# Performance work log

Hardware: AMD Instinct MI355X
Metric: run time of the kernel (lower is better)

Reference implementation:

```python
import jax, jax.numpy as jnp
import numpy as np

HEADS = 8
DIM_HEAD = 64
QUERY_DIM = 320
INNER = HEADS * DIM_HEAD
B = 1
N = 2304          # 48*48 latent pixels
HS = WS = 48
SCALE = DIM_HEAD ** -0.5
ATTN_MATRIX_SCALE = 1.5   # injection_config['T']


def setup_inputs() -> dict:
    key = jax.random.key(0)
    ks = jax.random.split(key, 10)
    f = lambda k, s: jax.random.normal(k, s, dtype=jnp.float32)
    return {
        'x': f(ks[0], (B, N, QUERY_DIM)),
        'Wq': f(ks[1], (QUERY_DIM, INNER)) * 0.05,
        'Wo': f(ks[2], (INNER, QUERY_DIM)) * 0.05,
        'bo': jnp.zeros((QUERY_DIM,), jnp.float32),
        'q_injected': f(ks[3], (B * HEADS, N, DIM_HEAD)),
        'k_injected': f(ks[4], (B * HEADS, N, DIM_HEAD)),
        'v_injected': f(ks[5], (B * HEADS, N, DIM_HEAD)),
        'cnt_k_injected': f(ks[6], (B * HEADS, N, DIM_HEAD)),
        'cnt_v_injected': f(ks[7], (B * HEADS, N, DIM_HEAD)),
        'mask': jax.random.uniform(ks[8], (HS, WS), dtype=jnp.float32),
    }


def _split_heads(t):
    # 'b n (h d) -> (b h) n d'
    b, n, _ = t.shape
    return t.reshape(b, n, HEADS, DIM_HEAD).transpose(0, 2, 1, 3).reshape(b * HEADS, n, DIM_HEAD)


def reference(x, Wq, Wo, bo, q_injected, k_injected, v_injected,
              cnt_k_injected, cnt_v_injected, mask):
    # --- q/k/v with injection (b=1 so torch.cat([.]*b) is identity) ---
    q_in = q_injected                          # (bh, N, d)
    q_ = _split_heads(x @ Wq)                  # to_q(x) -> (bh, N, d)
    q = 0.5 * q_in + 0.5 * q_                  # blended query
    k = k_injected
    v = v_injected
    q_cnt, k_cnt, v_cnt = q_in, cnt_k_injected, cnt_v_injected

    # --- get_batch_sim: content-content similarity (b=1 => rearrange is identity) ---
    cc_sim = jnp.einsum('hid,hjd->hij', q_cnt, k_cnt) * SCALE     # (h, N, N)

    # --- get_batch_sim_with_mask ---
    sim = jnp.einsum('hid,hjd->hij', q, k) * (ATTN_MATRIX_SCALE * SCALE)  # (h, N, N)
    sim_r = sim.reshape(HEADS, HS, WS, N)
    cc_r = cc_sim.reshape(HEADS, HS, WS, N)
    max_sim = jnp.einsum('hid,hjd->hij', q_cnt, k)                # delta_q x delta_k (=self.k)
    max_sim_r = max_sim.reshape(HEADS, HS, WS, N)
    min_cc = jnp.min(cc_r, axis=3, keepdims=True)                 # (h, HS, WS, 1)
    max_ms = jnp.max(max_sim_r, axis=3, keepdims=True)            # (h, HS, WS, 1)

    # binary-threshold the mask, flip sign, bilinear-resize to (HS, WS)
    m = jnp.where(mask < 0.5, -1.0, jnp.where(mask > 0.5, 1.0, mask)) * -1.0
    m = jax.image.resize(m[None, None], (1, 1, HS, WS), method='bilinear')
    m = m.reshape(1, HS, WS, 1)

    gvm = (min_cc - max_ms) * m                                   # gradual_vanished_mask
    sim = (sim_r + gvm).reshape(HEADS, N, N)                      # rows [:WS] == all rows here

    # B=1 => the view/permute/reshape block is identity: sim, cc_sim are (h, N, N)
    # concatenated softmax over style keys and content keys
    cat_sim = jnp.concatenate([sim, cc_sim], axis=2)              # (h, N, 2N)
    cat_attn = jax.nn.softmax(cat_sim, axis=-1)
    cat_v = jnp.concatenate([v, v_cnt], axis=1)                   # (h, 2N, d)
    cat_out = jnp.einsum('hij,hjd->hid', cat_attn, cat_v)         # (h, N, d)

    # 'h (b n) d -> b n (h d)' with b=1
    out = cat_out.transpose(1, 0, 2).reshape(B, N, INNER)
    return out @ Wo + bo
```

## Files before the change

kernel.cpp:

```cpp
#include <hip/hip_runtime.h>
#include <math.h>

#define HEADS 8
#define NTOK  2304
#define DH    64
#define QD    320
#define INNER 512
#define TPS   36
#define PSTR  68

typedef _Float16 f16;
typedef f16  f16x4 __attribute__((ext_vector_type(4)));
typedef f16  f16x8 __attribute__((ext_vector_type(8)));
typedef float f32x4 __attribute__((ext_vector_type(4)));

#define MFMA(a,b,c) __builtin_amdgcn_mfma_f32_16x16x32_f16((a),(b),(c),0,0,0)

#define GLDS(gp, lp) __builtin_amdgcn_global_load_lds(                      \
    (const __attribute__((address_space(1))) void*)(gp),                    \
    (__attribute__((address_space(3))) void*)(lp), 16, 0, 0)

#if __has_builtin(__builtin_amdgcn_exp2f)
#define EXP2(x) __builtin_amdgcn_exp2f(x)
#else
#define EXP2(x) exp2f(x)
#endif

#define LOG2E 1.44269504f

static __device__ __forceinline__ unsigned pkrtz(float a, float b) {
#if __has_builtin(__builtin_amdgcn_cvt_pkrtz)
  return __builtin_bit_cast(unsigned, __builtin_amdgcn_cvt_pkrtz(a, b));
#else
  union { f16 h[2]; unsigned u; } c;
  c.h[0] = (f16)a; c.h[1] = (f16)b;
  return c.u;
#endif
}

__global__ __launch_bounds__(256) void prep_all(
    const float* __restrict__ qi, const float* __restrict__ ki,
    const float* __restrict__ kc, const float* __restrict__ x,
    const float* __restrict__ v,  const float* __restrict__ vc,
    const float* __restrict__ Wq, const float* __restrict__ Wo,
    f16* __restrict__ oq, f16* __restrict__ ok, f16* __restrict__ okc,
    f16* __restrict__ ox, f16* __restrict__ vt, f16* __restrict__ vct,
    f16* __restrict__ WqT, f16* __restrict__ WoT)
{
  __shared__ float T[64][65];
  const int bid = blockIdx.x;
  const int tid = threadIdx.x;

  if (bid < 2088) {
    int i = bid * 256 + tid;
    const float* src; f16* dst; float s = 1.0f; int off;
    if (i < 147456)      { src = qi; dst = oq;  off = i; }
    else if (i < 294912) { src = ki; dst = ok;  off = i - 147456; }
    else if (i < 442368) { src = kc; dst = okc; off = i - 294912; s = 0.125f * LOG2E; }
    else                 { src = x;  dst = ox;  off = i - 442368; }
    float4 a = reinterpret_cast<const float4*>(src)[off * 2];
    float4 b = reinterpret_cast<const float4*>(src)[off * 2 + 1];
    f16x8 o;
    o[0] = (f16)(a.x * s); o[1] = (f16)(a.y * s);
    o[2] = (f16)(a.z * s); o[3] = (f16)(a.w * s);
    o[4] = (f16)(b.x * s); o[5] = (f16)(b.y * s);
    o[6] = (f16)(b.z * s); o[7] = (f16)(b.w * s);
    *reinterpret_cast<f16x8*>(&dst[(size_t)off * 8]) = o;
  } else if (bid < 2664) {
    int t = bid - 2088;
    int z = t / 288, rem = t % 288;
    int h = rem / 36, nt = rem % 36;
    const float* src = z ? vc : v;
    f16* dst = z ? vct : vt;
    const int n0 = nt * 64;
    const size_t base = ((size_t)h * NTOK + n0) * DH;
    for (int it = 0; it < 4; ++it) {
      int idx = tid + it * 256;
      int n = idx >> 4, d0 = (idx & 15) * 4;
      float4 a = *reinterpret_cast<const float4*>(&src[base + (size_t)n * DH + d0]);
      T[n][d0] = a.x; T[n][d0 + 1] = a.y; T[n][d0 + 2] = a.z; T[n][d0 + 3] = a.w;
    }
    __syncthreads();
    for (int it = 0; it < 2; ++it) {
      int idx = tid + it * 256;
      int d = idx >> 3, c0 = (idx & 7) * 8;
      f16x8 o;
      #pragma unroll
      for (int i = 0; i < 8; ++i) o[i] = (f16)T[c0 + i][d];
      *reinterpret_cast<f16x8*>(&dst[(size_t)(h * 64 + d) * NTOK + n0 + c0]) = o;
    }
  } else {
    int t = bid - 2664;
    int z = t / 40, b = t % 40;
    const float* src = z ? Wo : Wq;
    f16* dst = z ? WoT : WqT;
    const int R = z ? INNER : QD;
    const int C = z ? QD : INNER;
    const int ctiles = C >> 6;
    const int rt = b / ctiles, ct = b % ctiles;
    for (int it = 0; it < 4; ++it) {
      int idx = tid + it * 256;
      int r = idx >> 4, c4 = (idx & 15) * 4;
      float4 a = *reinterpret_cast<const float4*>(&src[(size_t)(rt * 64 + r) * C + ct * 64 + c4]);
      T[r][c4] = a.x; T[r][c4 + 1] = a.y; T[r][c4 + 2] = a.z; T[r][c4 + 3] = a.w;
    }
    __syncthreads();
    for (int it = 0; it < 4; ++it) {
      int idx = tid + it * 256;
      int c = idx >> 4, r4 = (idx & 15) * 4;
      f16x4 o;
      #pragma unroll
      for (int i = 0; i < 4; ++i) o[i] = (f16)T[r4 + i][c];
      *reinterpret_cast<f16x4*>(&dst[(size_t)(ct * 64 + c) * R + rt * 64 + r4]) = o;
    }
  }
}

__global__ __launch_bounds__(256) void qblend_mfma(
    const f16* __restrict__ x16, const f16* __restrict__ WqT,
    const float* __restrict__ qinj, f16* __restrict__ qhat)
{
  const int qt = blockIdx.x, h = blockIdx.y;
  const int n0 = qt * 32;
  const int tid = threadIdx.x;
  const int w = tid >> 6, l = tid & 63, lq = l & 15, lk = l >> 4;
  const int qsub = w & 1, ch = w >> 1;
  f32x4 acc[2] = {};
  const f16* arow = x16 + (size_t)(n0 + qsub * 16 + lq) * QD;
  #pragma unroll
  for (int ks = 0; ks < 10; ++ks) {
    f16x8 a = *reinterpret_cast<const f16x8*>(&arow[ks * 32 + lk * 8]);
    #pragma unroll
    for (int df = 0; df < 2; ++df) {
      const f16* brow = WqT + (size_t)(h * 64 + ch * 32 + df * 16 + lq) * QD;
      f16x8 b = *reinterpret_cast<const f16x8*>(&brow[ks * 32 + lk * 8]);
      acc[df] = MFMA(a, b, acc[df]);
    }
  }
  const float sc = 0.09375f * LOG2E;
  #pragma unroll
  for (int df = 0; df < 2; ++df)
    #pragma unroll
    for (int r = 0; r < 4; ++r) {
      int n = n0 + qsub * 16 + lk * 4 + r;
      int d = ch * 32 + df * 16 + lq;
      size_t idx = ((size_t)h * NTOK + n) * DH + d;
      qhat[idx] = (f16)(sc * (qinj[idx] + acc[df][r]));
    }
}

__global__ __launch_bounds__(64) void attn_pw(
    const f16* __restrict__ qhat, const f16* __restrict__ qc16,
    const f16* __restrict__ k16,  const f16* __restrict__ kc16,
    const f16* __restrict__ vt16, const f16* __restrict__ vct16,
    float* __restrict__ part)
{
  __shared__ __align__(16) f16 smem[3][2][2048];
  __shared__ __align__(16) f16 pbuf[640];

  const int bid = blockIdx.x;
  const int h    = bid & 7;
  const int strm = (bid >> 3) & 1;
  const int sp   = (bid >> 4) & 1;
  const int wq   = bid >> 5;
  const int l = threadIdx.x;
  const int lq = l & 15, lk = l >> 4;
  const size_t hb = (size_t)h * NTOK * DH;
  const int row0 = wq * 48 + lq;

  f16x8 qh0[2], qh1[2], qh2[2], qc0[2], qc1[2], qc2[2];
  {
    const size_t qr0 = hb + (size_t)row0 * DH;
    #pragma unroll
    for (int ks = 0; ks < 2; ++ks) {
      const int o = ks * 32 + lk * 8;
      qc0[ks] = *reinterpret_cast<const f16x8*>(&qc16[qr0 + o]);
      qc1[ks] = *reinterpret_cast<const f16x8*>(&qc16[qr0 + 16 * DH + o]);
      qc2[ks] = *reinterpret_cast<const f16x8*>(&qc16[qr0 + 32 * DH + o]);
      if (!strm) {
        qh0[ks] = *reinterpret_cast<const f16x8*>(&qhat[qr0 + o]);
        qh1[ks] = *reinterpret_cast<const f16x8*>(&qhat[qr0 + 16 * DH + o]);
        qh2[ks] = *reinterpret_cast<const f16x8*>(&qhat[qr0 + 32 * DH + o]);
      } else { qh0[ks] = qc0[ks]; qh1[ks] = qc1[ks]; qh2[ks] = qc2[ks]; }
    }
  }

  const int ksw  = ((l & 7) ^ (l >> 3)) * 8;
  const int krw  = l >> 3;
  const int vrw  = l >> 2;
  const int voff = (l & 3) * 8;
  const f16* gK = (strm ? kc16 : k16) + hb;
  const f16* gV = (strm ? vct16 : vt16) + (size_t)h * DH * NTOK;

  #define STAGE(nb, j0)                                                       \
    do {                                                                      \
      _Pragma("unroll")                                                       \
      for (int c = 0; c < 4; ++c) {                                           \
        GLDS(gK + (size_t)((j0) + c * 8 + krw) * 64 + ksw,                    \
             &smem[nb][0][c * 512]);                                          \
        GLDS(gV + (size_t)(c * 16 + vrw) * NTOK + (j0) + voff,                \
             &smem[nb][1][c * 512]);                                          \
      }                                                                       \
    } while (0)

  const int swz = (lq & 7) * 8;
  int xo[2];
  #pragma unroll
  for (int ks = 0; ks < 2; ++ks) xo[ks] = ((ks * 32 + lk * 8) ^ swz);

  float S0 = 0.f, S1 = 0.f, S2 = 0.f;
  float ax0, ax1, ax2;
  ax0 = ax1 = ax2 = strm ? INFINITY : -INFINITY;
  f32x4 O0[4] = {}, O1_[4] = {}, O2_[4] = {};

  auto SMX = [&](const f32x4* s, float& Sl) -> f16x8 {
    float p0 = EXP2(s[0][0]), p1 = EXP2(s[0][1]);
    float p2 = EXP2(s[0][2]), p3 = EXP2(s[0][3]);
    float p4 = EXP2(s[1][0]), p5 = EXP2(s[1][1]);
    float p6 = EXP2(s[1][2]), p7 = EXP2(s[1][3]);
    Sl += ((p0 + p1) + (p2 + p3)) + ((p4 + p5) + (p6 + p7));
    uint2 wA, wB;
    wA.x = pkrtz(p0, p1); wA.y = pkrtz(p2, p3);
    wB.x = pkrtz(p4, p5); wB.y = pkrtz(p6, p7);
    *reinterpret_cast<uint2*>(pbuf + lq * 40 + lk * 4)      = wA;
    *reinterpret_cast<uint2*>(pbuf + lq * 40 + 16 + lk * 4) = wB;
    return *reinterpret_cast<const f16x8*>(pbuf + lq * 40 + lk * 8);
  };

  const int jb = sp * (TPS * 32);
  STAGE(0, jb);
  STAGE(1, jb + 32);

  for (int t = 0; t < TPS; ++t) {
    if (t + 2 < TPS) {
      STAGE((t + 2) % 3, jb + (t + 2) * 32);
      asm volatile("s_waitcnt vmcnt(16)" ::: "memory");
    } else if (t + 1 < TPS) {
      asm volatile("s_waitcnt vmcnt(8)" ::: "memory");
    } else {
      asm volatile("s_waitcnt vmcnt(0)" ::: "memory");
    }
    __builtin_amdgcn_sched_barrier(0);

    const int bi = t % 3;
    const f16* Kb = &smem[bi][0][0];
    const f16* Vb = &smem[bi][1][0];

    f32x4 sA[2] = {}, sB[2] = {}, sC[2] = {};
    __builtin_amdgcn_s_setprio(1);
    if (!strm) {
      float m3A = -INFINITY, m3B = -INFINITY, m3C = -INFINITY;
      #pragma unroll
      for (int jf = 0; jf < 2; ++jf) {
        f32x4 tA = {}, tB = {}, tC = {};
        const int rb = (jf * 16 + lq) * 64;
        #pragma unroll
        for (int ks = 0; ks < 2; ++ks) {
          f16x8 aK = *reinterpret_cast<const f16x8*>(&Kb[rb + xo[ks]]);
          sA[jf] = MFMA(aK, qh0[ks], sA[jf]);
          sB[jf] = MFMA(aK, qh1[ks], sB[jf]);
          sC[jf] = MFMA(aK, qh2[ks], sC[jf]);
          tA = MFMA(aK, qc0[ks], tA);
          tB = MFMA(aK, qc1[ks], tB);
          tC = MFMA(aK, qc2[ks], tC);
        }
        m3A = fmaxf(m3A, fmaxf(fmaxf(tA[0], tA[1]), fmaxf(tA[2], tA[3])));
        m3B = fmaxf(m3B, fmaxf(fmaxf(tB[0], tB[1]), fmaxf(tB[2], tB[3])));
        m3C = fmaxf(m3C, fmaxf(fmaxf(tC[0], tC[1]), fmaxf(tC[2], tC[3])));
      }
      ax0 = fmaxf(ax0, m3A); ax1 = fmaxf(ax1, m3B); ax2 = fmaxf(ax2, m3C);
    } else {
      #pragma unroll
      for (int jf = 0; jf < 2; ++jf) {
        const int rb = (jf * 16 + lq) * 64;
        #pragma unroll
        for (int ks = 0; ks < 2; ++ks) {
          f16x8 aK = *reinterpret_cast<const f16x8*>(&Kb[rb + xo[ks]]);
          sA[jf] = MFMA(aK, qc0[ks], sA[jf]);
          sB[jf] = MFMA(aK, qc1[ks], sB[jf]);
          sC[jf] = MFMA(aK, qc2[ks], sC[jf]);
        }
      }
      ax0 = fminf(ax0, fminf(fminf(fminf(sA[0][0], sA[0][1]), fminf(sA[0][2], sA[0][3])),
                             fminf(fminf(sA[1][0], sA[1][1]), fminf(sA[1][2], sA[1][3]))));
      ax1 = fminf(ax1, fminf(fminf(fminf(sB[0][0], sB[0][1]), fminf(sB[0][2], sB[0][3])),
                             fminf(fminf(sB[1][0], sB[1][1]), fminf(sB[1][2], sB[1][3]))));
      ax2 = fminf(ax2, fminf(fminf(fminf(sC[0][0], sC[0][1]), fminf(sC[0][2], sC[0][3])),
                             fminf(fminf(sC[1][0], sC[1][1]), fminf(sC[1][2], sC[1][3]))));
    }
    __builtin_amdgcn_s_setprio(0);

    f16x8 pbA = SMX(sA, S0);
    f16x8 pbB = SMX(sB, S1);
    f16x8 pbC = SMX(sC, S2);

    __builtin_amdgcn_s_setprio(1);
    #pragma unroll
    for (int df = 0; df < 4; ++df) {
      f16x8 aV = *reinterpret_cast<const f16x8*>(&Vb[(df * 16 + lq) * 32 + lk * 8]);
      O0[df]  = MFMA(aV, pbA, O0[df]);
      O1_[df] = MFMA(aV, pbB, O1_[df]);
      O2_[df] = MFMA(aV, pbC, O2_[df]);
    }
    __builtin_amdgcn_s_setprio(0);
  }

  S0 += __shfl_xor(S0, 16); S0 += __shfl_xor(S0, 32);
  S1 += __shfl_xor(S1, 16); S1 += __shfl_xor(S1, 32);
  S2 += __shfl_xor(S2, 16); S2 += __shfl_xor(S2, 32);
  if (!strm) {
    ax0 = fmaxf(ax0, __shfl_xor(ax0, 16)); ax0 = fmaxf(ax0, __shfl_xor(ax0, 32));
    ax1 = fmaxf(ax1, __shfl_xor(ax1, 16)); ax1 = fmaxf(ax1, __shfl_xor(ax1, 32));
    ax2 = fmaxf(ax2, __shfl_xor(ax2, 16)); ax2 = fmaxf(ax2, __shfl_xor(ax2, 32));
  } else {
    ax0 = fminf(ax0, __shfl_xor(ax0, 16)); ax0 = fminf(ax0, __shfl_xor(ax0, 32));
    ax1 = fminf(ax1, __shfl_xor(ax1, 16)); ax1 = fminf(ax1, __shfl_xor(ax1, 32));
    ax2 = fminf(ax2, __shfl_xor(ax2, 16)); ax2 = fminf(ax2, __shfl_xor(ax2, 32));
  }
  {
    const size_t u = (size_t)((strm * 2 + sp) * 8 + h);
    float* p0 = part + (u * NTOK + (size_t)row0) * PSTR;
    float* p1 = p0 + (size_t)16 * PSTR;
    float* p2 = p0 + (size_t)32 * PSTR;
    #pragma unroll
    for (int df = 0; df < 4; ++df) {
      *reinterpret_cast<f32x4*>(p0 + df * 16 + lk * 4) = O0[df];
      *reinterpret_cast<f32x4*>(p1 + df * 16 + lk * 4) = O1_[df];
      *reinterpret_cast<f32x4*>(p2 + df * 16 + lk * 4) = O2_[df];
    }
    if (lk == 0) {
      p0[64] = S0; p0[65] = ax0;
      p1[64] = S1; p1[65] = ax1;
      p2[64] = S2; p2[65] = ax2;
    }
  }
  #undef STAGE
}

__global__ __launch_bounds__(256) void merge4(
    const float* __restrict__ part, const float* __restrict__ mask,
    f16* __restrict__ mid)
{
  const int qt = blockIdx.x, h = blockIdx.y;
  const int tid = threadIdx.x;
  const int r = tid >> 2, ds = (tid & 3) * 16;
  const int n = qt * 64 + r;
  const float* pA0 = part + ((size_t)(0  + h) * NTOK + n) * PSTR;
  const float* pA1 = part + ((size_t)(8  + h) * NTOK + n) * PSTR;
  const float* pB0 = part + ((size_t)(16 + h) * NTOK + n) * PSTR;
  const float* pB1 = part + ((size_t)(24 + h) * NTOK + n) * PSTR;

  float S1 = pA0[64] + pA1[64];
  float S2 = pB0[64] + pB1[64];
  float mx = fmaxf(pA0[65], pA1[65]);
  float mn = fminf(pB0[65], pB1[65]);

  float mv = mask[n];
  float mm = (mv < 0.5f) ? 1.0f : (mv > 0.5f ? -1.0f : -mv);
  float gvm = (mn - mx * LOG2E) * mm;
  float A1 = gvm;
  float Mf = fmaxf(A1, 0.0f);
  float w1 = exp2f(A1 - Mf), w2 = exp2f(-Mf);
  float inv = 1.0f / (w1 * S1 + w2 * S2);

  f16 ov[16];
  #pragma unroll
  for (int c = 0; c < 4; ++c) {
    float4 o1a = *reinterpret_cast<const float4*>(pA0 + ds + c * 4);
    float4 o1b = *reinterpret_cast<const float4*>(pA1 + ds + c * 4);
    float4 o2a = *reinterpret_cast<const float4*>(pB0 + ds + c * 4);
    float4 o2b = *reinterpret_cast<const float4*>(pB1 + ds + c * 4);
    ov[c*4+0] = (f16)((w1 * (o1a.x + o1b.x) + w2 * (o2a.x + o2b.x)) * inv);
    ov[c*4+1] = (f16)((w1 * (o1a.y + o1b.y) + w2 * (o2a.y + o2b.y)) * inv);
    ov[c*4+2] = (f16)((w1 * (o1a.z + o1b.z) + w2 * (o2a.z + o2b.z)) * inv);
    ov[c*4+3] = (f16)((w1 * (o1a.w + o1b.w) + w2 * (o2a.w + o2b.w)) * inv);
  }
  f16* dst = mid + (size_t)n * INNER + h * 64 + ds;
  *reinterpret_cast<f16x8*>(dst)     = *reinterpret_cast<f16x8*>(&ov[0]);
  *reinterpret_cast<f16x8*>(dst + 8) = *reinterpret_cast<f16x8*>(&ov[8]);
}

__global__ __launch_bounds__(64) void out_mfma(
    const f16* __restrict__ mid, const f16* __restrict__ WoT,
    const float* __restrict__ bo, float* __restrict__ out)
{
  const int n0 = blockIdx.x * 16;
  const int o0 = blockIdx.y * 64;
  const int l = threadIdx.x, lq = l & 15, lk = l >> 4;
  f32x4 acc[4] = {};
  const f16* arow = mid + (size_t)(n0 + lq) * INNER;
  #pragma unroll
  for (int ks = 0; ks < 16; ++ks) {
    f16x8 a = *reinterpret_cast<const f16x8*>(&arow[ks * 32 + lk * 8]);
    #pragma unroll
    for (int df = 0; df < 4; ++df) {
      f16x8 b = *reinterpret_cast<const f16x8*>(
          &WoT[(size_t)(o0 + df * 16 + lq) * INNER + ks * 32 + lk * 8]);
      acc[df] = MFMA(a, b, acc[df]);
    }
  }
  #pragma unroll
  for (int df = 0; df < 4; ++df) {
    float bb = bo[o0 + df * 16 + lq];
    #pragma unroll
    for (int r = 0; r < 4; ++r) {
      int n = n0 + lk * 4 + r;
      out[(size_t)n * QD + o0 + df * 16 + lq] = acc[df][r] + bb;
    }
  }
}

extern "C" void kernel_launch(void* const* d_in, const int* in_sizes, int n_in,
                              void* d_out, int out_size, void* d_ws, size_t ws_size,
                              hipStream_t stream) {
  const float* x    = (const float*)d_in[0];
  const float* Wq   = (const float*)d_in[1];
  const float* Wo   = (const float*)d_in[2];
  const float* bo   = (const float*)d_in[3];
  const float* qinj = (const float*)d_in[4];
  const float* kinj = (const float*)d_in[5];
  const float* vinj = (const float*)d_in[6];
  const float* kcnt = (const float*)d_in[7];
  const float* vcnt = (const float*)d_in[8];
  const float* mask = (const float*)d_in[9];
  float* out = (float*)d_out;

  const size_t T = (size_t)HEADS * NTOK * DH;
  f16* qhat = (f16*)d_ws;
  f16* qc16 = qhat + T;
  f16* k16  = qc16 + T;
  f16* kc16 = k16  + T;
  f16* vt16 = kc16 + T;
  f16* vct16= vt16 + T;
  f16* mid  = vct16 + T;
  f16* x16  = mid;
  f16* WqT  = mid + 737280;
  f16* WoT  = mid + T;
  float* part = (float*)(WoT + 163840);

  prep_all   <<<2744, 256, 0, stream>>>(qinj, kinj, kcnt, x, vinj, vcnt, Wq, Wo,
                                        qc16, k16, kc16, x16, vt16, vct16, WqT, WoT);
  qblend_mfma<<<dim3(72, 8), 256, 0, stream>>>(x16, WqT, qinj, qhat);
  attn_pw    <<<1536, 64, 0, stream>>>(qhat, qc16, k16, kc16, vt16, vct16, part);
  merge4     <<<dim3(36, 8), 256, 0, stream>>>(part, mask, mid);
  out_mfma   <<<dim3(144, 5), 64, 0, stream>>>(mid, WoT, bo, out);
}
```

Before: 96.37 us.

## Merge key-split partials inside a two-wave block via LDS instead of global

```diff
diff --git a/kernel.cpp b/kernel.cpp
--- a/kernel.cpp
+++ b/kernel.cpp
@@ -149,21 +149,21 @@
     }
 }
 
-__global__ __launch_bounds__(64) void attn_pw(
+__global__ __launch_bounds__(128, 2) void attn_ib(
     const f16* __restrict__ qhat, const f16* __restrict__ qc16,
     const f16* __restrict__ k16,  const f16* __restrict__ kc16,
     const f16* __restrict__ vt16, const f16* __restrict__ vct16,
     float* __restrict__ part)
 {
-  __shared__ __align__(16) f16 smem[3][2][2048];
-  __shared__ __align__(16) f16 pbuf[640];
+  __shared__ __align__(16) f16 smemF[24576];
+  __shared__ __align__(16) f16 pbuf[2][640];
 
   const int bid = blockIdx.x;
   const int h    = bid & 7;
   const int strm = (bid >> 3) & 1;
-  const int sp   = (bid >> 4) & 1;
-  const int wq   = bid >> 5;
-  const int l = threadIdx.x;
+  const int wq   = bid >> 4;
+  const int tid = threadIdx.x;
+  const int w = tid >> 6, l = tid & 63;
   const int lq = l & 15, lk = l >> 4;
   const size_t hb = (size_t)h * NTOK * DH;
   const int row0 = wq * 48 + lq;
@@ -185,33 +185,36 @@
     }
   }
 
-  const int ksw  = ((l & 7) ^ (l >> 3)) * 8;
-  const int krw  = l >> 3;
-  const int vrw  = l >> 2;
-  const int voff = (l & 3) * 8;
+  const int krw = l >> 3;
+  const int ksw = ((l & 7) ^ (l >> 3)) * 8;
+  const int vrw = l >> 2;
+  const int vsw = ((l & 3) ^ ((l >> 3) & 3)) * 8;
   const f16* gK = (strm ? kc16 : k16) + hb;
   const f16* gV = (strm ? vct16 : vt16) + (size_t)h * DH * NTOK;
-
-  #define STAGE(nb, j0)                                                       \
-    do {                                                                      \
-      _Pragma("unroll")                                                       \
-      for (int c = 0; c < 4; ++c) {                                           \
-        GLDS(gK + (size_t)((j0) + c * 8 + krw) * 64 + ksw,                    \
-             &smem[nb][0][c * 512]);                                          \
-        GLDS(gV + (size_t)(c * 16 + vrw) * NTOK + (j0) + voff,                \
-             &smem[nb][1][c * 512]);                                          \
-      }                                                                       \
+  const int wbase = __builtin_amdgcn_readfirstlane(w * 12288);
+
+  #define STAGE(nb, j0)                                                      \
+    do {                                                                     \
+      _Pragma("unroll")                                                      \
+      for (int c = 0; c < 4; ++c) {                                          \
+        GLDS(gK + (size_t)((j0) + c * 8 + krw) * 64 + ksw,                   \
+             &smemF[wbase + (nb) * 4096 + c * 512]);                         \
+        GLDS(gV + (size_t)(c * 16 + vrw) * NTOK + (j0) + vsw,                \
+             &smemF[wbase + (nb) * 4096 + 2048 + c * 512]);                  \
+      }                                                                      \
     } while (0)
 
   const int swz = (lq & 7) * 8;
   int xo[2];
   #pragma unroll
   for (int ks = 0; ks < 2; ++ks) xo[ks] = ((ks * 32 + lk * 8) ^ swz);
+  const int vxo = (lk ^ ((lq >> 1) & 3)) * 8;
 
   float S0 = 0.f, S1 = 0.f, S2 = 0.f;
   float ax0, ax1, ax2;
   ax0 = ax1 = ax2 = strm ? INFINITY : -INFINITY;
   f32x4 O0[4] = {}, O1_[4] = {}, O2_[4] = {};
+  f16* Pq = &pbuf[w][0];
 
   auto SMX = [&](const f32x4* s, float& Sl) -> f16x8 {
     float p0 = EXP2(s[0][0]), p1 = EXP2(s[0][1]);
@@ -222,12 +225,12 @@
     uint2 wA, wB;
     wA.x = pkrtz(p0, p1); wA.y = pkrtz(p2, p3);
     wB.x = pkrtz(p4, p5); wB.y = pkrtz(p6, p7);
-    *reinterpret_cast<uint2*>(pbuf + lq * 40 + lk * 4)      = wA;
-    *reinterpret_cast<uint2*>(pbuf + lq * 40 + 16 + lk * 4) = wB;
-    return *reinterpret_cast<const f16x8*>(pbuf + lq * 40 + lk * 8);
+    *reinterpret_cast<uint2*>(Pq + lq * 40 + lk * 4)      = wA;
+    *reinterpret_cast<uint2*>(Pq + lq * 40 + 16 + lk * 4) = wB;
+    return *reinterpret_cast<const f16x8*>(Pq + lq * 40 + lk * 8);
   };
 
-  const int jb = sp * (TPS * 32);
+  const int jb = w * (TPS * 32);
   STAGE(0, jb);
   STAGE(1, jb + 32);
 
@@ -243,8 +246,8 @@
     __builtin_amdgcn_sched_barrier(0);
 
     const int bi = t % 3;
-    const f16* Kb = &smem[bi][0][0];
-    const f16* Vb = &smem[bi][1][0];
+    const f16* Kb = &smemF[wbase + bi * 4096];
+    const f16* Vb = Kb + 2048;
 
     f32x4 sA[2] = {}, sB[2] = {}, sC[2] = {};
     __builtin_amdgcn_s_setprio(1);
@@ -297,7 +300,7 @@
     __builtin_amdgcn_s_setprio(1);
     #pragma unroll
     for (int df = 0; df < 4; ++df) {
-      f16x8 aV = *reinterpret_cast<const f16x8*>(&Vb[(df * 16 + lq) * 32 + lk * 8]);
+      f16x8 aV = *reinterpret_cast<const f16x8*>(&Vb[(df * 16 + lq) * 32 + vxo]);
       O0[df]  = MFMA(aV, pbA, O0[df]);
       O1_[df] = MFMA(aV, pbB, O1_[df]);
       O2_[df] = MFMA(aV, pbC, O2_[df]);
@@ -305,20 +308,52 @@
     __builtin_amdgcn_s_setprio(0);
   }
 
-  S0 += __shfl_xor(S0, 16); S0 += __shfl_xor(S0, 32);
-  S1 += __shfl_xor(S1, 16); S1 += __shfl_xor(S1, 32);
-  S2 += __shfl_xor(S2, 16); S2 += __shfl_xor(S2, 32);
-  if (!strm) {
-    ax0 = fmaxf(ax0, __shfl_xor(ax0, 16)); ax0 = fmaxf(ax0, __shfl_xor(ax0, 32));
-    ax1 = fmaxf(ax1, __shfl_xor(ax1, 16)); ax1 = fmaxf(ax1, __shfl_xor(ax1, 32));
-    ax2 = fmaxf(ax2, __shfl_xor(ax2, 16)); ax2 = fmaxf(ax2, __shfl_xor(ax2, 32));
-  } else {
-    ax0 = fminf(ax0, __shfl_xor(ax0, 16)); ax0 = fminf(ax0, __shfl_xor(ax0, 32));
-    ax1 = fminf(ax1, __shfl_xor(ax1, 16)); ax1 = fminf(ax1, __shfl_xor(ax1, 32));
-    ax2 = fminf(ax2, __shfl_xor(ax2, 16)); ax2 = fminf(ax2, __shfl_xor(ax2, 32));
-  }
-  {
-    const size_t u = (size_t)((strm * 2 + sp) * 8 + h);
+  float* mrg = reinterpret_cast<float*>(&smemF[0]);
+  __syncthreads();
+  if (w == 1) {
+    #pragma unroll
+    for (int df = 0; df < 4; ++df) {
+      *reinterpret_cast<f32x4*>(mrg + 0 * 1024 + l * 16 + df * 4) = O0[df];
+      *reinterpret_cast<f32x4*>(mrg + 1 * 1024 + l * 16 + df * 4) = O1_[df];
+      *reinterpret_cast<f32x4*>(mrg + 2 * 1024 + l * 16 + df * 4) = O2_[df];
+    }
+    mrg[3072 + (0 * 64 + l) * 2] = S0; mrg[3072 + (0 * 64 + l) * 2 + 1] = ax0;
+    mrg[3072 + (1 * 64 + l) * 2] = S1; mrg[3072 + (1 * 64 + l) * 2 + 1] = ax1;
+    mrg[3072 + (2 * 64 + l) * 2] = S2; mrg[3072 + (2 * 64 + l) * 2 + 1] = ax2;
+  }
+  __syncthreads();
+  if (w == 0) {
+    #pragma unroll
+    for (int df = 0; df < 4; ++df) {
+      O0[df]  += *reinterpret_cast<const f32x4*>(mrg + 0 * 1024 + l * 16 + df * 4);
+      O1_[df] += *reinterpret_cast<const f32x4*>(mrg + 1 * 1024 + l * 16 + df * 4);
+      O2_[df] += *reinterpret_cast<const f32x4*>(mrg + 2 * 1024 + l * 16 + df * 4);
+    }
+    S0 += mrg[3072 + (0 * 64 + l) * 2];
+    S1 += mrg[3072 + (1 * 64 + l) * 2];
+    S2 += mrg[3072 + (2 * 64 + l) * 2];
+    if (!strm) {
+      ax0 = fmaxf(ax0, mrg[3072 + (0 * 64 + l) * 2 + 1]);
+      ax1 = fmaxf(ax1, mrg[3072 + (1 * 64 + l) * 2 + 1]);
+      ax2 = fmaxf(ax2, mrg[3072 + (2 * 64 + l) * 2 + 1]);
+    } else {
+      ax0 = fminf(ax0, mrg[3072 + (0 * 64 + l) * 2 + 1]);
+      ax1 = fminf(ax1, mrg[3072 + (1 * 64 + l) * 2 + 1]);
+      ax2 = fminf(ax2, mrg[3072 + (2 * 64 + l) * 2 + 1]);
+    }
+    S0 += __shfl_xor(S0, 16); S0 += __shfl_xor(S0, 32);
+    S1 += __shfl_xor(S1, 16); S1 += __shfl_xor(S1, 32);
+    S2 += __shfl_xor(S2, 16); S2 += __shfl_xor(S2, 32);
+    if (!strm) {
+      ax0 = fmaxf(ax0, __shfl_xor(ax0, 16)); ax0 = fmaxf(ax0, __shfl_xor(ax0, 32));
+      ax1 = fmaxf(ax1, __shfl_xor(ax1, 16)); ax1 = fmaxf(ax1, __shfl_xor(ax1, 32));
+      ax2 = fmaxf(ax2, __shfl_xor(ax2, 16)); ax2 = fmaxf(ax2, __shfl_xor(ax2, 32));
+    } else {
+      ax0 = fminf(ax0, __shfl_xor(ax0, 16)); ax0 = fminf(ax0, __shfl_xor(ax0, 32));
+      ax1 = fminf(ax1, __shfl_xor(ax1, 16)); ax1 = fminf(ax1, __shfl_xor(ax1, 32));
+      ax2 = fminf(ax2, __shfl_xor(ax2, 16)); ax2 = fminf(ax2, __shfl_xor(ax2, 32));
+    }
+    const size_t u = (size_t)(strm * 8 + h);
     float* p0 = part + (u * NTOK + (size_t)row0) * PSTR;
     float* p1 = p0 + (size_t)16 * PSTR;
     float* p2 = p0 + (size_t)32 * PSTR;
@@ -337,7 +372,7 @@
   #undef STAGE
 }
 
-__global__ __launch_bounds__(256) void merge4(
+__global__ __launch_bounds__(256) void merge2s(
     const float* __restrict__ part, const float* __restrict__ mask,
     f16* __restrict__ mid)
 {
@@ -345,15 +380,12 @@
   const int tid = threadIdx.x;
   const int r = tid >> 2, ds = (tid & 3) * 16;
   const int n = qt * 64 + r;
-  const float* pA0 = part + ((size_t)(0  + h) * NTOK + n) * PSTR;
-  const float* pA1 = part + ((size_t)(8  + h) * NTOK + n) * PSTR;
-  const float* pB0 = part + ((size_t)(16 + h) * NTOK + n) * PSTR;
-  const float* pB1 = part + ((size_t)(24 + h) * NTOK + n) * PSTR;
-
-  float S1 = pA0[64] + pA1[64];
-  float S2 = pB0[64] + pB1[64];
-  float mx = fmaxf(pA0[65], pA1[65]);
-  float mn = fminf(pB0[65], pB1[65]);
+  const float* pA = part + ((size_t)(0 + h) * NTOK + n) * PSTR;
+  const float* pB = part + ((size_t)(8 + h) * NTOK + n) * PSTR;
+
+  float S1 = pA[64], S2 = pB[64];
+  float mx = pA[65];
+  float mn = pB[65];
 
   float mv = mask[n];
   float mm = (mv < 0.5f) ? 1.0f : (mv > 0.5f ? -1.0f : -mv);
@@ -366,14 +398,12 @@
   f16 ov[16];
   #pragma unroll
   for (int c = 0; c < 4; ++c) {
-    float4 o1a = *reinterpret_cast<const float4*>(pA0 + ds + c * 4);
-    float4 o1b = *reinterpret_cast<const float4*>(pA1 + ds + c * 4);
-    float4 o2a = *reinterpret_cast<const float4*>(pB0 + ds + c * 4);
-    float4 o2b = *reinterpret_cast<const float4*>(pB1 + ds + c * 4);
-    ov[c*4+0] = (f16)((w1 * (o1a.x + o1b.x) + w2 * (o2a.x + o2b.x)) * inv);
-    ov[c*4+1] = (f16)((w1 * (o1a.y + o1b.y) + w2 * (o2a.y + o2b.y)) * inv);
-    ov[c*4+2] = (f16)((w1 * (o1a.z + o1b.z) + w2 * (o2a.z + o2b.z)) * inv);
-    ov[c*4+3] = (f16)((w1 * (o1a.w + o1b.w) + w2 * (o2a.w + o2b.w)) * inv);
+    float4 o1 = *reinterpret_cast<const float4*>(pA + ds + c * 4);
+    float4 o2 = *reinterpret_cast<const float4*>(pB + ds + c * 4);
+    ov[c*4+0] = (f16)((w1 * o1.x + w2 * o2.x) * inv);
+    ov[c*4+1] = (f16)((w1 * o1.y + w2 * o2.y) * inv);
+    ov[c*4+2] = (f16)((w1 * o1.z + w2 * o2.z) * inv);
+    ov[c*4+3] = (f16)((w1 * o1.w + w2 * o2.w) * inv);
   }
   f16* dst = mid + (size_t)n * INNER + h * 64 + ds;
   *reinterpret_cast<f16x8*>(dst)     = *reinterpret_cast<f16x8*>(&ov[0]);
@@ -441,7 +471,7 @@
   prep_all   <<<2744, 256, 0, stream>>>(qinj, kinj, kcnt, x, vinj, vcnt, Wq, Wo,
                                         qc16, k16, kc16, x16, vt16, vct16, WqT, WoT);
   qblend_mfma<<<dim3(72, 8), 256, 0, stream>>>(x16, WqT, qinj, qhat);
-  attn_pw    <<<1536, 64, 0, stream>>>(qhat, qc16, k16, kc16, vt16, vct16, part);
-  merge4     <<<dim3(36, 8), 256, 0, stream>>>(part, mask, mid);
+  attn_ib    <<<768, 128, 0, stream>>>(qhat, qc16, k16, kc16, vt16, vct16, part);
+  merge2s    <<<dim3(36, 8), 256, 0, stream>>>(part, mask, mid);
   out_mfma   <<<dim3(144, 5), 64, 0, stream>>>(mid, WoT, bo, out);
 }
```

Result: faster. 85.40 us (-11.4%).
